# Kernel tuning notes

Hardware: AMD Instinct MI355X
Metric: run time of the kernel (lower is better)

The kernel has to match this reference:

```python
import jax, jax.numpy as jnp
import numpy as np

# dims: B batch, C tokens-per-patch, S num_patches, T input_channel(=output_channel), D d_model, P pool_size
B, C, S, T, D, P = 8, 512, 64, 128, 256, 8
EPS = 1e-5


def _cos_attn(pooled, keys):
    # pooled: (B,S,F), keys: (P,F) -> softmax over pool of cosine similarities: (B,S,P)
    pn = pooled / (jnp.linalg.norm(pooled, axis=-1, keepdims=True) + 1e-8)
    kn = keys / (jnp.linalg.norm(keys, axis=-1, keepdims=True) + 1e-8)
    return jax.nn.softmax(jnp.einsum('bsf,pf->bsp', pn, kn), axis=-1)


def setup_inputs() -> dict:
    key = jax.random.key(0)
    ks = jax.random.split(key, 5)
    sc = lambda k, shape, fan: jax.random.normal(k, shape, jnp.float32) * np.float32(1.0 / np.sqrt(fan))
    return {
        'x': jax.random.normal(ks[0], (B, C, S, T), jnp.float32),
        'gamma': jnp.ones((T,), jnp.float32),
        'beta': jnp.zeros((T,), jnp.float32),
        'keys1': sc(ks[1], (P, T), T),      # routing keys, WeightPool1
        'Wp1': sc(ks[2], (P, D, T), T),     # weight bank, T -> D
        'bp1': jnp.zeros((P, D), jnp.float32),
        'keys2': sc(ks[3], (P, D), D),      # routing keys, WeightPool2
        'Wp2': sc(ks[4], (P, T, D), D),     # weight bank, D -> T
        'bp2': jnp.zeros((P, T), jnp.float32),
    }


def reference(x, gamma, beta, keys1, Wp1, bp1, keys2, Wp2, bp2):
    # x_proj = Identity(x) since input_channel == output_channel
    # BatchNorm2d over channel T (x permuted to (B,T,S,C)) == normalize x over dims (0,1,2)
    mean = x.mean(axis=(0, 1, 2))
    var = x.var(axis=(0, 1, 2))  # biased, as torch BN training stats
    y = (x - mean) * jax.lax.rsqrt(var + EPS) * gamma + beta  # (B,C,S,T)

    # WeightPool1: pool over C, cosine-route into weight bank
    a1 = _cos_attn(y.mean(axis=1), keys1)            # (B,S,P)
    w1 = jnp.einsum('bsp,pdt->bsdt', a1, Wp1)        # (B,S,D,T)
    b1 = jnp.einsum('bsp,pd->bsd', a1, bp1)          # (B,S,D)

    y = jnp.einsum('bcst,bsdt->bcsd', y, w1) + b1[:, None]  # (B,C,S,D)
    y = jax.nn.relu(y)
    # dropout: inference mode (identity)

    # WeightPool2
    a2 = _cos_attn(y.mean(axis=1), keys2)            # (B,S,P)
    w2 = jnp.einsum('bsp,ptd->bstd', a2, Wp2)        # (B,S,T,D)
    b2 = jnp.einsum('bsp,pt->bst', a2, bp2)          # (B,S,T)

    y = jnp.einsum('bcsd,bstd->bcst', y, w2) + b2[:, None]  # (B,C,S,T)
    return (x + y, w1, w2)
```

## Files before the change

### kernel.cpp

```cpp
#include <hip/hip_runtime.h>
#include <hip/hip_bf16.h>

#define BB 8
#define CC 512
#define SS 64
#define TT 128
#define DD 256
#define PP 8
#define BS (BB*SS)
#define NSTAT (BB*CC*SS)
#define EPSV 1e-5f

typedef float f32x4 __attribute__((ext_vector_type(4)));
typedef __bf16 bf16x8 __attribute__((ext_vector_type(8)));

__device__ __forceinline__ unsigned short f2bf(float f) {
  unsigned u = __float_as_uint(f);
  u += 0x7FFFu + ((u >> 16) & 1u);
  return (unsigned short)(u >> 16);
}
__device__ __forceinline__ float bf2f(unsigned short h) {
  return __uint_as_float(((unsigned)h) << 16);
}

__global__ __launch_bounds__(256) void k1_stats(const float* __restrict__ x,
    float* __restrict__ csum_part, float* __restrict__ ssq_part,
    unsigned short* __restrict__ xbf) {
  int bid = blockIdx.x;
  int bs = bid >> 2, cq = bid & 3;
  int b = bs >> 6, s = bs & 63;
  const float* xb = x + ((size_t)b * CC * SS + s) * TT;
  unsigned short* xo = xbf + ((size_t)b * CC * SS + s) * TT;
  int tid = threadIdx.x;
  int t4 = tid & 31, coff = tid >> 5;
  float cs0=0,cs1=0,cs2=0,cs3=0, ss0=0,ss1=0,ss2=0,ss3=0;
  #pragma unroll 8
  for (int k = 0; k < 16; k++) {
    int c = cq*128 + coff + k*8;
    float4 v = *reinterpret_cast<const float4*>(xb + (size_t)c*(SS*TT) + t4*4);
    ushort4 o; o.x=f2bf(v.x); o.y=f2bf(v.y); o.z=f2bf(v.z); o.w=f2bf(v.w);
    *reinterpret_cast<ushort4*>(xo + (size_t)c*(SS*TT) + t4*4) = o;
    cs0 += v.x; cs1 += v.y; cs2 += v.z; cs3 += v.w;
    ss0 += v.x*v.x; ss1 += v.y*v.y; ss2 += v.z*v.z; ss3 += v.w*v.w;
  }
  __shared__ float4 redC[256];
  __shared__ float4 redS[256];
  redC[tid] = make_float4(cs0,cs1,cs2,cs3);
  redS[tid] = make_float4(ss0,ss1,ss2,ss3);
  __syncthreads();
  if (tid < 32) {
    #pragma unroll
    for (int j = 1; j < 8; j++) {
      float4 a = redC[tid + j*32], bq = redS[tid + j*32];
      cs0+=a.x; cs1+=a.y; cs2+=a.z; cs3+=a.w;
      ss0+=bq.x; ss1+=bq.y; ss2+=bq.z; ss3+=bq.w;
    }
    int t0 = tid*4;
    csum_part[(size_t)(t0+0)*2048 + bid] = cs0;
    csum_part[(size_t)(t0+1)*2048 + bid] = cs1;
    csum_part[(size_t)(t0+2)*2048 + bid] = cs2;
    csum_part[(size_t)(t0+3)*2048 + bid] = cs3;
    ssq_part[(size_t)(t0+0)*2048 + bid] = ss0;
    ssq_part[(size_t)(t0+1)*2048 + bid] = ss1;
    ssq_part[(size_t)(t0+2)*2048 + bid] = ss2;
    ssq_part[(size_t)(t0+3)*2048 + bid] = ss3;
  }
}

__global__ __launch_bounds__(256) void k1b_reduce(
    const float* __restrict__ csum_part, const float* __restrict__ ssq_part,
    float* __restrict__ sumt, float* __restrict__ sumsq) {
  int t = blockIdx.x, tid = threadIdx.x;
  const float* cp = csum_part + (size_t)t*2048;
  const float* sp = ssq_part + (size_t)t*2048;
  float cs = 0.f, ss = 0.f;
  #pragma unroll
  for (int k=0;k<8;k++) { cs += cp[tid + k*256]; ss += sp[tid + k*256]; }
  #pragma unroll
  for (int off=32; off; off>>=1) { cs += __shfl_xor(cs,off); ss += __shfl_xor(ss,off); }
  __shared__ float redc[4], reds[4];
  int wave = tid >> 6, lane = tid & 63;
  if (lane == 0) { redc[wave] = cs; reds[wave] = ss; }
  __syncthreads();
  if (tid == 0) {
    sumt[t]  = redc[0]+redc[1]+redc[2]+redc[3];
    sumsq[t] = reds[0]+reds[1]+reds[2]+reds[3];
  }
}

__global__ __launch_bounds__(256) void k2_route1(
    const float* __restrict__ sumt, const float* __restrict__ sumsq,
    const float* __restrict__ csum_part, const float* __restrict__ gamma,
    const float* __restrict__ beta, const float* __restrict__ keys1,
    const float* __restrict__ Wp1, const float* __restrict__ bp1,
    float* __restrict__ w1out, unsigned short* __restrict__ w1bf,
    float* __restrict__ b1) {
  int bid = blockIdx.x;
  int bs = bid >> 2, q = bid & 3;
  int tid = threadIdx.x;
  __shared__ float a1s[PP];
  __shared__ float g_s[TT], h_s[TT];
  __shared__ float db_s[64];
  if (tid < TT) {
    float m = sumt[tid] * (1.f/NSTAT);
    float var = sumsq[tid]*(1.f/NSTAT) - m*m;
    float g = gamma[tid] * rsqrtf(var + EPSV);
    g_s[tid] = g;
    h_s[tid] = beta[tid] - m*g;
  }
  if (tid < 64) {
    float pv0, pv1;
    {
      int t = tid;
      float4 c4v = *reinterpret_cast<const float4*>(csum_part + (size_t)t*2048 + bs*4);
      float cs = c4v.x + c4v.y + c4v.z + c4v.w;
      float m = sumt[t] * (1.f/NSTAT);
      float var = sumsq[t]*(1.f/NSTAT) - m*m;
      float g = gamma[t] * rsqrtf(var + EPSV);
      pv0 = (cs*(1.f/CC) - m)*g + beta[t];
    }
    {
      int t = tid + 64;
      float4 c4v = *reinterpret_cast<const float4*>(csum_part + (size_t)t*2048 + bs*4);
      float cs = c4v.x + c4v.y + c4v.z + c4v.w;
      float m = sumt[t] * (1.f/NSTAT);
      float var = sumsq[t]*(1.f/NSTAT) - m*m;
      float g = gamma[t] * rsqrtf(var + EPSV);
      pv1 = (cs*(1.f/CC) - m)*g + beta[t];
    }
    float ssq = pv0*pv0 + pv1*pv1;
    #pragma unroll
    for (int off=32; off; off>>=1) ssq += __shfl_xor(ssq, off);
    float pn = sqrtf(ssq) + 1e-8f;
    float lg[PP];
    #pragma unroll
    for (int p=0;p<PP;p++) {
      float k0 = keys1[p*TT + tid], k1 = keys1[p*TT + tid + 64];
      float dot = pv0*k0 + pv1*k1;
      float kn = k0*k0 + k1*k1;
      #pragma unroll
      for (int off=32; off; off>>=1) { dot += __shfl_xor(dot,off); kn += __shfl_xor(kn,off); }
      lg[p] = dot / (pn * (sqrtf(kn) + 1e-8f));
    }
    if (tid == 0) {
      float mx = lg[0];
      #pragma unroll
      for (int p=1;p<PP;p++) mx = fmaxf(mx, lg[p]);
      float se = 0.f, e[PP];
      #pragma unroll
      for (int p=0;p<PP;p++){ e[p] = __expf(lg[p]-mx); se += e[p]; }
      float inv = 1.f/se;
      #pragma unroll
      for (int p=0;p<PP;p++) a1s[p] = e[p]*inv;
    }
  }
  __syncthreads();
  float a[PP];
  #pragma unroll
  for (int p=0;p<PP;p++) a[p]=a1s[p];
  #pragma unroll
  for (int i=0;i<8;i++) {
    int idx = tid + i*256;
    int dr = idx >> 5, c4 = idx & 31;
    size_t roff = (size_t)(q*64+dr)*TT + c4*4;
    size_t off = (size_t)bs*(DD*TT) + roff;
    float4 accv = make_float4(0.f,0.f,0.f,0.f);
    #pragma unroll
    for (int p=0;p<PP;p++) {
      float4 v = *reinterpret_cast<const float4*>(Wp1 + (size_t)p*(DD*TT) + roff);
      accv.x += a[p]*v.x; accv.y += a[p]*v.y; accv.z += a[p]*v.z; accv.w += a[p]*v.w;
    }
    *reinterpret_cast<float4*>(w1out + off) = accv;
    float4 gv = *reinterpret_cast<const float4*>(g_s + c4*4);
    ushort4 o;
    o.x=f2bf(accv.x*gv.x); o.y=f2bf(accv.y*gv.y);
    o.z=f2bf(accv.z*gv.z); o.w=f2bf(accv.w*gv.w);
    *reinterpret_cast<ushort4*>(w1bf + off) = o;
    float4 hv = *reinterpret_cast<const float4*>(h_s + c4*4);
    float pd = accv.x*hv.x + accv.y*hv.y + accv.z*hv.z + accv.w*hv.w;
    #pragma unroll
    for (int off2=16; off2; off2>>=1) pd += __shfl_xor(pd, off2);
    if (c4 == 0) db_s[dr] = pd;
  }
  __syncthreads();
  if (tid < 64) {
    int d = q*64 + tid;
    float bacc = db_s[tid];
    #pragma unroll
    for (int p=0;p<PP;p++) bacc += a[p]*bp1[p*DD + d];
    b1[(size_t)bs*DD + d] = bacc;
  }
}

__global__ __launch_bounds__(512) void k3_gemm1(
    const unsigned short* __restrict__ xbf, const unsigned short* __restrict__ w1bf,
    const float* __restrict__ b1, unsigned short* __restrict__ zbf,
    float* __restrict__ p2part) {
  int bid = blockIdx.x;
  int bs = bid >> 2, mt = bid & 3;
  int b = bs >> 6, s = bs & 63;
  __shared__ unsigned short lA[128*128];
  __shared__ unsigned short lB[256*128];
  int tid = threadIdx.x;
  char* lAc = reinterpret_cast<char*>(lA);
  char* lBc = reinterpret_cast<char*>(lB);
  const unsigned short* xb = xbf + (((size_t)b*CC + mt*128)*SS + s)*TT;
  #pragma unroll
  for (int i=0;i<4;i++) {
    int flat = tid + i*512;
    int r = flat >> 4, c8 = flat & 15;
    uint4 v = *reinterpret_cast<const uint4*>(xb + (size_t)r*(SS*TT) + c8*8);
    unsigned addr = (unsigned)(r*256) + (((unsigned)(c8*16)) ^ (((unsigned)(r&7))<<4));
    *reinterpret_cast<uint4*>(lAc + addr) = v;
  }
  const unsigned short* wsrc = w1bf + (size_t)bs*(DD*TT);
  #pragma unroll
  for (int i=0;i<8;i++) {
    int flat = tid + i*512;
    int n = flat >> 4, ch = flat & 15;
    uint4 v = *reinterpret_cast<const uint4*>(wsrc + (size_t)flat*8);
    unsigned addr = (unsigned)(n*256) + (((unsigned)(ch*16)) ^ (((unsigned)(n&7))<<4));
    *reinterpret_cast<uint4*>(lBc + addr) = v;
  }
  __syncthreads();
  int wave = tid >> 6, lane = tid & 63;
  int wm = wave >> 2, wn = wave & 3;
  int lr = lane & 15, kg = lane >> 4;
  f32x4 zero = {0.f,0.f,0.f,0.f};
  f32x4 acc[4][4];
  #pragma unroll
  for (int m=0;m<4;m++)
    #pragma unroll
    for (int n=0;n<4;n++) acc[m][n] = zero;
  #pragma unroll
  for (int k0=0;k0<128;k0+=32) {
    bf16x8 af[4], bfr[4];
    #pragma unroll
    for (int m=0;m<4;m++) {
      int row = wm*64 + m*16 + lr;
      unsigned addr = (unsigned)(row*256) + (((unsigned)(k0*2 + kg*16)) ^ (((unsigned)(row&7))<<4));
      af[m] = *reinterpret_cast<const bf16x8*>(lAc + addr);
    }
    #pragma unroll
    for (int n=0;n<4;n++) {
      int row = wn*64 + n*16 + lr;
      unsigned addr = (unsigned)(row*256) + (((unsigned)(k0*2 + kg*16)) ^ (((unsigned)(row&7))<<4));
      bfr[n] = *reinterpret_cast<const bf16x8*>(lBc + addr);
    }
    #pragma unroll
    for (int m=0;m<4;m++)
      #pragma unroll
      for (int n=0;n<4;n++)
        acc[m][n] = __builtin_amdgcn_mfma_f32_16x16x32_bf16(af[m], bfr[n], acc[m][n], 0, 0, 0);
  }
  const float* b1p = b1 + (size_t)bs*DD;
  float* p2p = p2part + (((size_t)bid*2) + wm)*DD;
  __syncthreads();
  #pragma unroll
  for (int n=0;n<4;n++) {
    int d = wn*64 + n*16 + lr;
    float bv = b1p[d];
    float csum = 0.f;
    #pragma unroll
    for (int m=0;m<4;m++) {
      int rbase = wm*64 + m*16 + kg*4;
      #pragma unroll
      for (int j=0;j<4;j++) {
        float v = fmaxf(acc[m][n][j] + bv, 0.f);
        lB[(rbase+j)*DD + d] = f2bf(v);
        csum += v;
      }
    }
    csum += __shfl_xor(csum, 16);
    csum += __shfl_xor(csum, 32);
    if (kg == 0) p2p[d] = csum;
  }
  __syncthreads();
  unsigned short* zb = zbf + (((size_t)b*CC + mt*128)*SS + s)*DD;
  #pragma unroll
  for (int i=0;i<8;i++) {
    int flat = tid + i*512;
    int r = flat >> 5, ch = flat & 31;
    uint4 v = *reinterpret_cast<const uint4*>(lBc + flat*16);
    *reinterpret_cast<uint4*>(zb + (size_t)r*(SS*DD) + ch*8) = v;
  }
}

__global__ __launch_bounds__(256) void k4_route2(
    const float* __restrict__ p2part, const float* __restrict__ keys2,
    const float* __restrict__ Wp2, const float* __restrict__ bp2,
    float* __restrict__ w2out, unsigned short* __restrict__ w2bf,
    float* __restrict__ b2) {
  int bid = blockIdx.x;
  int bs = bid >> 2, q = bid & 3;
  int tid = threadIdx.x;
  __shared__ float a2s[PP];
  if (tid < 64) {
    float pv[4]; float ssq = 0.f;
    #pragma unroll
    for (int j=0;j<4;j++) {
      int d = tid + 64*j;
      float s8 = 0.f;
      #pragma unroll
      for (int r=0;r<8;r++) s8 += p2part[((size_t)bs*8 + r)*DD + d];
      pv[j] = s8 * (1.f/CC);
      ssq += pv[j]*pv[j];
    }
    #pragma unroll
    for (int off=32; off; off>>=1) ssq += __shfl_xor(ssq, off);
    float pn = sqrtf(ssq) + 1e-8f;
    float lg[PP];
    #pragma unroll
    for (int p=0;p<PP;p++) {
      float dot = 0.f, kn = 0.f;
      #pragma unroll
      for (int j=0;j<4;j++) {
        int d = tid + 64*j;
        float kv = keys2[p*DD + d];
        dot += pv[j]*kv; kn += kv*kv;
      }
      #pragma unroll
      for (int off=32; off; off>>=1) { dot += __shfl_xor(dot,off); kn += __shfl_xor(kn,off); }
      lg[p] = dot / (pn * (sqrtf(kn)+1e-8f));
    }
    if (tid == 0) {
      float mx = lg[0];
      #pragma unroll
      for (int p=1;p<PP;p++) mx = fmaxf(mx,lg[p]);
      float se=0.f, e[PP];
      #pragma unroll
      for (int p=0;p<PP;p++){ e[p]=__expf(lg[p]-mx); se+=e[p]; }
      float inv = 1.f/se;
      #pragma unroll
      for (int p=0;p<PP;p++) a2s[p]=e[p]*inv;
    }
  }
  __syncthreads();
  float a[PP];
  #pragma unroll
  for (int p=0;p<PP;p++) a[p]=a2s[p];
  #pragma unroll
  for (int i=0;i<8;i++) {
    int idx = tid + i*256;
    int tr = idx >> 6, c4 = idx & 63;
    size_t roff = (size_t)(q*32+tr)*DD + c4*4;
    size_t off = (size_t)bs*(TT*DD) + roff;
    float4 accv = make_float4(0.f,0.f,0.f,0.f);
    #pragma unroll
    for (int p=0;p<PP;p++) {
      float4 v = *reinterpret_cast<const float4*>(Wp2 + (size_t)p*(TT*DD) + roff);
      accv.x += a[p]*v.x; accv.y += a[p]*v.y; accv.z += a[p]*v.z; accv.w += a[p]*v.w;
    }
    *reinterpret_cast<float4*>(w2out + off) = accv;
    ushort4 o; o.x=f2bf(accv.x); o.y=f2bf(accv.y); o.z=f2bf(accv.z); o.w=f2bf(accv.w);
    *reinterpret_cast<ushort4*>(w2bf + off) = o;
  }
  if (tid < 32) {
    int t = q*32 + tid;
    float bacc = 0.f;
    #pragma unroll
    for (int p=0;p<PP;p++) bacc += a[p]*bp2[p*TT + t];
    b2[(size_t)bs*TT + t] = bacc;
  }
}

__global__ __launch_bounds__(1024, 4) void k5_gemm2(
    const unsigned short* __restrict__ zbf, const unsigned short* __restrict__ w2bf,
    const float* __restrict__ b2, const unsigned short* __restrict__ xbf,
    float* __restrict__ out) {
  int bid = blockIdx.x;
  int bs = bid >> 2, mt = bid & 3;
  int b = bs >> 6, s = bs & 63;
  __shared__ unsigned short lA[128*256];
  __shared__ unsigned short lB[128*256];
  int tid = threadIdx.x;
  char* lAc = reinterpret_cast<char*>(lA);
  char* lBc = reinterpret_cast<char*>(lB);
  const unsigned short* za = zbf + (((size_t)b*CC + mt*128)*SS + s)*DD;
  #pragma unroll
  for (int i=0;i<4;i++) {
    int flat = tid + i*1024;
    int r = flat >> 5, ch = flat & 31;
    uint4 v = *reinterpret_cast<const uint4*>(za + (size_t)r*(SS*DD) + ch*8);
    unsigned addr = (unsigned)(r*512) + (((unsigned)(ch*16)) ^ (((unsigned)(r&7))<<4));
    *reinterpret_cast<uint4*>(lAc + addr) = v;
  }
  const unsigned short* wsrc = w2bf + (size_t)bs*(TT*DD);
  #pragma unroll
  for (int i=0;i<4;i++) {
    int flat = tid + i*1024;
    int r = flat >> 5, ch = flat & 31;
    uint4 v = *reinterpret_cast<const uint4*>(wsrc + (size_t)flat*8);
    unsigned addr = (unsigned)(r*512) + (((unsigned)(ch*16)) ^ (((unsigned)(r&7))<<4));
    *reinterpret_cast<uint4*>(lBc + addr) = v;
  }
  __syncthreads();
  int wave = tid >> 6, lane = tid & 63;
  int wm = wave >> 2, wn = wave & 3;
  int lr = lane & 15, kg = lane >> 4;
  f32x4 zero = {0.f,0.f,0.f,0.f};
  f32x4 acc[2][2];
  #pragma unroll
  for (int m=0;m<2;m++)
    #pragma unroll
    for (int n=0;n<2;n++) acc[m][n] = zero;
  #pragma unroll
  for (int k0=0;k0<256;k0+=32) {
    bf16x8 af[2], bfr[2];
    #pragma unroll
    for (int m=0;m<2;m++) {
      int row = wm*32 + m*16 + lr;
      unsigned addr = (unsigned)(row*512) + (((unsigned)(k0*2 + kg*16)) ^ (((unsigned)(row&7))<<4));
      af[m] = *reinterpret_cast<const bf16x8*>(lAc + addr);
    }
    #pragma unroll
    for (int n=0;n<2;n++) {
      int row = wn*32 + n*16 + lr;
      unsigned addr = (unsigned)(row*512) + (((unsigned)(k0*2 + kg*16)) ^ (((unsigned)(row&7))<<4));
      bfr[n] = *reinterpret_cast<const bf16x8*>(lBc + addr);
    }
    #pragma unroll
    for (int m=0;m<2;m++)
      #pragma unroll
      for (int n=0;n<2;n++)
        acc[m][n] = __builtin_amdgcn_mfma_f32_16x16x32_bf16(af[m], bfr[n], acc[m][n], 0, 0, 0);
  }
  const float* b2p = b2 + (size_t)bs*TT;
  const unsigned short* xb = xbf + (((size_t)b*CC + mt*128)*SS + s)*TT;
  float* ob = out + (((size_t)b*CC + mt*128)*SS + s)*TT;
  #pragma unroll
  for (int n=0;n<2;n++) {
    int t = wn*32 + n*16 + lr;
    float bv = b2p[t];
    #pragma unroll
    for (int m=0;m<2;m++) {
      int rbase = wm*32 + m*16 + kg*4;
      #pragma unroll
      for (int j=0;j<4;j++) {
        size_t off = (size_t)(rbase+j)*(SS*TT) + t;
        ob[off] = acc[m][n][j] + bv + bf2f(xb[off]);
      }
    }
  }
}

extern "C" void kernel_launch(void* const* d_in, const int* in_sizes, int n_in,
                              void* d_out, int out_size, void* d_ws, size_t ws_size,
                              hipStream_t stream) {
  (void)in_sizes; (void)n_in; (void)out_size; (void)ws_size;
  const float* x     = (const float*)d_in[0];
  const float* gamma = (const float*)d_in[1];
  const float* beta  = (const float*)d_in[2];
  const float* keys1 = (const float*)d_in[3];
  const float* Wp1   = (const float*)d_in[4];
  const float* bp1   = (const float*)d_in[5];
  const float* keys2 = (const float*)d_in[6];
  const float* Wp2   = (const float*)d_in[7];
  const float* bp2   = (const float*)d_in[8];
  float* out = (float*)d_out;
  char* ws = (char*)d_ws;

  float* sumt        = (float*)(ws + 0);
  float* sumsq       = (float*)(ws + 512);
  float* csum_part   = (float*)(ws + 1024);
  float* ssq_part    = (float*)(ws + 1049600);
  float* p2part      = (float*)(ws + 2098176);
  float* b1          = (float*)(ws + 6292480);
  float* b2          = (float*)(ws + 6816768);
  unsigned short* w1bf = (unsigned short*)(ws + 7078912);
  unsigned short* w2bf = (unsigned short*)(ws + 40633344);
  unsigned short* xbf  = (unsigned short*)(ws + 74187776);
  unsigned short* zbf  = (unsigned short*)(ws + 141296640);

  float* w1out = out + 33554432;
  float* w2out = out + 50331648;

  k1_stats  <<<BS*4, 256,  0, stream>>>(x, csum_part, ssq_part, xbf);
  k1b_reduce<<<TT,   256,  0, stream>>>(csum_part, ssq_part, sumt, sumsq);
  k2_route1 <<<BS*4, 256,  0, stream>>>(sumt, sumsq, csum_part, gamma, beta, keys1, Wp1, bp1,
                                        w1out, w1bf, b1);
  k3_gemm1  <<<BS*4, 512,  0, stream>>>(xbf, w1bf, b1, zbf, p2part);
  k4_route2 <<<BS*4, 256,  0, stream>>>(p2part, keys2, Wp2, bp2, w2out, w2bf, b2);
  k5_gemm2  <<<BS*4, 1024, 0, stream>>>(zbf, w2bf, b2, xbf, out);
}
```

Before: 293.9 us.

## Recompute GEMM1 inside GEMM2 kernel instead of materializing Z intermediate

```diff
diff --git a/kernel.cpp b/kernel.cpp
--- a/kernel.cpp
+++ b/kernel.cpp
@@ -192,10 +192,9 @@
   }
 }
 
-__global__ __launch_bounds__(512) void k3_gemm1(
+__global__ __launch_bounds__(512) void k3_pool(
     const unsigned short* __restrict__ xbf, const unsigned short* __restrict__ w1bf,
-    const float* __restrict__ b1, unsigned short* __restrict__ zbf,
-    float* __restrict__ p2part) {
+    const float* __restrict__ b1, float* __restrict__ p2part) {
   int bid = blockIdx.x;
   int bs = bid >> 2, mt = bid & 3;
   int b = bs >> 6, s = bs & 63;
@@ -255,7 +254,6 @@
   }
   const float* b1p = b1 + (size_t)bs*DD;
   float* p2p = p2part + (((size_t)bid*2) + wm)*DD;
-  __syncthreads();
   #pragma unroll
   for (int n=0;n<4;n++) {
     int d = wn*64 + n*16 + lr;
@@ -263,26 +261,14 @@
     float csum = 0.f;
     #pragma unroll
     for (int m=0;m<4;m++) {
-      int rbase = wm*64 + m*16 + kg*4;
       #pragma unroll
       for (int j=0;j<4;j++) {
-        float v = fmaxf(acc[m][n][j] + bv, 0.f);
-        lB[(rbase+j)*DD + d] = f2bf(v);
-        csum += v;
+        csum += fmaxf(acc[m][n][j] + bv, 0.f);
       }
     }
     csum += __shfl_xor(csum, 16);
     csum += __shfl_xor(csum, 32);
     if (kg == 0) p2p[d] = csum;
-  }
-  __syncthreads();
-  unsigned short* zb = zbf + (((size_t)b*CC + mt*128)*SS + s)*DD;
-  #pragma unroll
-  for (int i=0;i<8;i++) {
-    int flat = tid + i*512;
-    int r = flat >> 5, ch = flat & 31;
-    uint4 v = *reinterpret_cast<const uint4*>(lBc + flat*16);
-    *reinterpret_cast<uint4*>(zb + (size_t)r*(SS*DD) + ch*8) = v;
   }
 }
 
@@ -364,81 +350,144 @@
   }
 }
 
-__global__ __launch_bounds__(1024, 4) void k5_gemm2(
-    const unsigned short* __restrict__ zbf, const unsigned short* __restrict__ w2bf,
-    const float* __restrict__ b2, const unsigned short* __restrict__ xbf,
-    float* __restrict__ out) {
+__global__ __launch_bounds__(1024, 4) void k5_fused(
+    const unsigned short* __restrict__ xbf, const unsigned short* __restrict__ w1bf,
+    const unsigned short* __restrict__ w2bf, const float* __restrict__ b1,
+    const float* __restrict__ b2, float* __restrict__ out) {
   int bid = blockIdx.x;
   int bs = bid >> 2, mt = bid & 3;
   int b = bs >> 6, s = bs & 63;
-  __shared__ unsigned short lA[128*256];
-  __shared__ unsigned short lB[128*256];
+  __shared__ __align__(16) char smem[163840];
+  char* lX  = smem;
+  char* lW  = smem + 32768;
+  char* lW2 = smem + 98304;
   int tid = threadIdx.x;
-  char* lAc = reinterpret_cast<char*>(lA);
-  char* lBc = reinterpret_cast<char*>(lB);
-  const unsigned short* za = zbf + (((size_t)b*CC + mt*128)*SS + s)*DD;
+  const unsigned short* xb  = xbf  + (((size_t)b*CC + mt*128)*SS + s)*TT;
+  const unsigned short* w1p = w1bf + (size_t)bs*(DD*TT);
+  const unsigned short* w2p = w2bf + (size_t)bs*(TT*DD);
+  #pragma unroll
+  for (int i=0;i<2;i++) {
+    int flat = tid + i*1024;
+    int r = flat >> 4, ch = flat & 15;
+    uint4 v = *reinterpret_cast<const uint4*>(xb + (size_t)r*(SS*TT) + ch*8);
+    unsigned addr = (unsigned)(r*256) + (((unsigned)(ch*16)) ^ (((unsigned)(r&7))<<4));
+    *reinterpret_cast<uint4*>(lX + addr) = v;
+  }
+  #pragma unroll
+  for (int i=0;i<4;i++) {
+    int flat = tid + i*1024;
+    int r = flat >> 4, ch = flat & 15;
+    uint4 v = *reinterpret_cast<const uint4*>(w1p + (size_t)flat*8);
+    unsigned addr = (unsigned)(r*256) + (((unsigned)(ch*16)) ^ (((unsigned)(r&7))<<4));
+    *reinterpret_cast<uint4*>(lW + addr) = v;
+  }
+  uint4 tw2[4];
+  #pragma unroll
+  for (int i=0;i<4;i++) {
+    int flat = tid + i*1024;
+    tw2[i] = *reinterpret_cast<const uint4*>(w2p + (size_t)flat*8);
+  }
+  int wave = tid >> 6, lane = tid & 63;
+  int lr = lane & 15, kg = lane >> 4;
+  int wm1 = wave >> 3, wn1 = wave & 7;
+  const float* b1p = b1 + (size_t)bs*DD;
+  float b1v0 = b1p[wn1*32 + 0*16 + lr];
+  float b1v1 = b1p[wn1*32 + 1*16 + lr];
+  __syncthreads();
+  f32x4 zero = {0.f,0.f,0.f,0.f};
+  f32x4 acc1[4][2];
+  #pragma unroll
+  for (int m=0;m<4;m++)
+    #pragma unroll
+    for (int n=0;n<2;n++) acc1[m][n] = zero;
+  #pragma unroll
+  for (int k0=0;k0<128;k0+=32) {
+    bf16x8 af[4], bfr[2];
+    #pragma unroll
+    for (int m=0;m<4;m++) {
+      int row = wm1*64 + m*16 + lr;
+      unsigned addr = (unsigned)(row*256) + (((unsigned)(k0*2 + kg*16)) ^ (((unsigned)(row&7))<<4));
+      af[m] = *reinterpret_cast<const bf16x8*>(lX + addr);
+    }
+    #pragma unroll
+    for (int n=0;n<2;n++) {
+      int row = wn1*32 + n*16 + lr;
+      unsigned addr = (unsigned)(row*256) + (((unsigned)(k0*2 + kg*16)) ^ (((unsigned)(row&7))<<4));
+      bfr[n] = *reinterpret_cast<const bf16x8*>(lW + addr);
+    }
+    #pragma unroll
+    for (int m=0;m<4;m++)
+      #pragma unroll
+      for (int n=0;n<2;n++)
+        acc1[m][n] = __builtin_amdgcn_mfma_f32_16x16x32_bf16(af[m], bfr[n], acc1[m][n], 0, 0, 0);
+  }
   #pragma unroll
   for (int i=0;i<4;i++) {
     int flat = tid + i*1024;
     int r = flat >> 5, ch = flat & 31;
-    uint4 v = *reinterpret_cast<const uint4*>(za + (size_t)r*(SS*DD) + ch*8);
     unsigned addr = (unsigned)(r*512) + (((unsigned)(ch*16)) ^ (((unsigned)(r&7))<<4));
-    *reinterpret_cast<uint4*>(lAc + addr) = v;
-  }
-  const unsigned short* wsrc = w2bf + (size_t)bs*(TT*DD);
-  #pragma unroll
-  for (int i=0;i<4;i++) {
-    int flat = tid + i*1024;
-    int r = flat >> 5, ch = flat & 31;
-    uint4 v = *reinterpret_cast<const uint4*>(wsrc + (size_t)flat*8);
-    unsigned addr = (unsigned)(r*512) + (((unsigned)(ch*16)) ^ (((unsigned)(r&7))<<4));
-    *reinterpret_cast<uint4*>(lBc + addr) = v;
-  }
-  __syncthreads();
-  int wave = tid >> 6, lane = tid & 63;
-  int wm = wave >> 2, wn = wave & 3;
-  int lr = lane & 15, kg = lane >> 4;
-  f32x4 zero = {0.f,0.f,0.f,0.f};
-  f32x4 acc[2][2];
+    *reinterpret_cast<uint4*>(lW2 + addr) = tw2[i];
+  }
+  __syncthreads();
+  #pragma unroll
+  for (int n=0;n<2;n++) {
+    int d = wn1*32 + n*16 + lr;
+    float bv = (n == 0) ? b1v0 : b1v1;
+    #pragma unroll
+    for (int m=0;m<4;m++) {
+      int rbase = wm1*64 + m*16 + kg*4;
+      #pragma unroll
+      for (int j=0;j<4;j++) {
+        int row = rbase + j;
+        float v = fmaxf(acc1[m][n][j] + bv, 0.f);
+        unsigned addr = (unsigned)(row*512) + (((unsigned)(d*2)) ^ (((unsigned)(row&7))<<4));
+        *reinterpret_cast<unsigned short*>(lW + addr) = f2bf(v);
+      }
+    }
+  }
+  __syncthreads();
+  int wm2 = wave >> 2, wn2 = wave & 3;
+  f32x4 acc2[2][2];
   #pragma unroll
   for (int m=0;m<2;m++)
     #pragma unroll
-    for (int n=0;n<2;n++) acc[m][n] = zero;
+    for (int n=0;n<2;n++) acc2[m][n] = zero;
   #pragma unroll
   for (int k0=0;k0<256;k0+=32) {
     bf16x8 af[2], bfr[2];
     #pragma unroll
     for (int m=0;m<2;m++) {
-      int row = wm*32 + m*16 + lr;
+      int row = wm2*32 + m*16 + lr;
       unsigned addr = (unsigned)(row*512) + (((unsigned)(k0*2 + kg*16)) ^ (((unsigned)(row&7))<<4));
-      af[m] = *reinterpret_cast<const bf16x8*>(lAc + addr);
+      af[m] = *reinterpret_cast<const bf16x8*>(lW + addr);
     }
     #pragma unroll
     for (int n=0;n<2;n++) {
-      int row = wn*32 + n*16 + lr;
+      int row = wn2*32 + n*16 + lr;
       unsigned addr = (unsigned)(row*512) + (((unsigned)(k0*2 + kg*16)) ^ (((unsigned)(row&7))<<4));
-      bfr[n] = *reinterpret_cast<const bf16x8*>(lBc + addr);
+      bfr[n] = *reinterpret_cast<const bf16x8*>(lW2 + addr);
     }
     #pragma unroll
     for (int m=0;m<2;m++)
       #pragma unroll
       for (int n=0;n<2;n++)
-        acc[m][n] = __builtin_amdgcn_mfma_f32_16x16x32_bf16(af[m], bfr[n], acc[m][n], 0, 0, 0);
+        acc2[m][n] = __builtin_amdgcn_mfma_f32_16x16x32_bf16(af[m], bfr[n], acc2[m][n], 0, 0, 0);
   }
   const float* b2p = b2 + (size_t)bs*TT;
-  const unsigned short* xb = xbf + (((size_t)b*CC + mt*128)*SS + s)*TT;
   float* ob = out + (((size_t)b*CC + mt*128)*SS + s)*TT;
   #pragma unroll
   for (int n=0;n<2;n++) {
-    int t = wn*32 + n*16 + lr;
+    int t = wn2*32 + n*16 + lr;
     float bv = b2p[t];
     #pragma unroll
     for (int m=0;m<2;m++) {
-      int rbase = wm*32 + m*16 + kg*4;
+      int rbase = wm2*32 + m*16 + kg*4;
       #pragma unroll
       for (int j=0;j<4;j++) {
-        size_t off = (size_t)(rbase+j)*(SS*TT) + t;
-        ob[off] = acc[m][n][j] + bv + bf2f(xb[off]);
+        int row = rbase + j;
+        unsigned xaddr = (unsigned)(row*256) + (((unsigned)(t*2)) ^ (((unsigned)(row&7))<<4));
+        float xv = bf2f(*reinterpret_cast<const unsigned short*>(lX + xaddr));
+        ob[(size_t)row*(SS*TT) + t] = acc2[m][n][j] + bv + xv;
       }
     }
   }
@@ -470,7 +519,6 @@
   unsigned short* w1bf = (unsigned short*)(ws + 7078912);
   unsigned short* w2bf = (unsigned short*)(ws + 40633344);
   unsigned short* xbf  = (unsigned short*)(ws + 74187776);
-  unsigned short* zbf  = (unsigned short*)(ws + 141296640);
 
   float* w1out = out + 33554432;
   float* w2out = out + 50331648;
@@ -479,7 +527,7 @@
   k1b_reduce<<<TT,   256,  0, stream>>>(csum_part, ssq_part, sumt, sumsq);
   k2_route1 <<<BS*4, 256,  0, stream>>>(sumt, sumsq, csum_part, gamma, beta, keys1, Wp1, bp1,
                                         w1out, w1bf, b1);
-  k3_gemm1  <<<BS*4, 512,  0, stream>>>(xbf, w1bf, b1, zbf, p2part);
+  k3_pool   <<<BS*4, 512,  0, stream>>>(xbf, w1bf, b1, p2part);
   k4_route2 <<<BS*4, 256,  0, stream>>>(p2part, keys2, Wp2, bp2, w2out, w2bf, b2);
-  k5_gemm2  <<<BS*4, 1024, 0, stream>>>(zbf, w2bf, b2, xbf, out);
-}
+  k5_fused  <<<BS*4, 1024, 0, stream>>>(xbf, w1bf, w2bf, b1, b2, out);
+}
```

New measurement: 307.4 us. 4.6% more time.
